# Kernel optimization log

Hardware: AMD Instinct MI355X
Metric: run time of the kernel (lower is better)

The kernel has to match this reference:

```python
import jax, jax.numpy as jnp
import numpy as np

EPS = 1e-12


def setup_inputs() -> dict:
    key = jax.random.key(0)
    k1, k2, k3 = jax.random.split(key, 3)
    N, D, K = 262144, 64, 1024
    input_data = jax.random.normal(k1, (N, D), dtype=jnp.float32)
    random_vector = jax.random.normal(k2, (N, D), dtype=jnp.float32)
    # HeUniform over (K, D): limit = sqrt(6 / fan_in) with fan_in = K
    limit = np.sqrt(6.0 / K)
    codebooks = jax.random.uniform(k3, (K, D), dtype=jnp.float32, minval=-limit, maxval=limit)
    codebooks_used = jnp.zeros((K,), dtype=jnp.int32)
    return {"input_data": input_data, "random_vector": random_vector,
            "codebooks": codebooks, "codebooks_used": codebooks_used}


def reference(input_data, random_vector, codebooks, codebooks_used):
    # training=True path of NSVQ.call
    K = codebooks.shape[0]
    N = input_data.shape[0]
    sim = input_data @ codebooks.T
    dists = (jnp.sum(input_data * input_data, axis=1, keepdims=True)
             + jnp.sum(codebooks * codebooks, axis=1)[None, :]
             - 2.0 * sim)
    min_indices = jnp.argmin(dists, axis=1)                      # [N]
    hard_q = codebooks[min_indices]                              # [N, D]
    # NSVQ noise substitution
    res_norm = jnp.sqrt(jnp.sum((input_data - hard_q) ** 2, axis=1, keepdims=True))
    rv_norm = jnp.sqrt(jnp.sum(random_vector ** 2, axis=1, keepdims=True))
    vq_error = (res_norm / (rv_norm + EPS)) * random_vector
    quantized_input = input_data + vq_error
    # perplexity from code usage histogram
    counts = jax.ops.segment_sum(jnp.ones((N,), dtype=jnp.float32), min_indices,
                                 num_segments=K)                 # [K]
    avg_probs = counts / jnp.float32(N)
    perplexity = jnp.exp(-jnp.sum(avg_probs * jnp.log(avg_probs + EPS)))
    codebooks_used_new = codebooks_used + counts.astype(jnp.int32)
    return quantized_input, perplexity, codebooks_used_new
```

## Files before the change

### kernel.cpp

```cpp
#include <hip/hip_runtime.h>
#include <math.h>


#define NROWS 262144
#define DIM 64
#define KCODES 1024
#define ND ((size_t)NROWS * DIM)

typedef __attribute__((ext_vector_type(8))) _Float16 f16x8;
typedef __attribute__((ext_vector_type(4))) float f32x4;

typedef const __attribute__((address_space(1))) void* as1p;
typedef __attribute__((address_space(3))) void* as3p;
__device__ inline void gl_lds16(const void* g, void* l) {
    __builtin_amdgcn_global_load_lds((as1p)g, (as3p)l, 16, 0, 0);
}

__global__ __launch_bounds__(256) void nsvq_prep(
    const float* __restrict__ cb, _Float16* __restrict__ cbs,
    float* __restrict__ cnorm)
{
    const int tid = blockIdx.x * 256 + threadIdx.x;
    const int k = tid >> 3;
    const int u = tid & 7;
    const float* p = cb + (size_t)k * DIM + u * 8;
    float4 f0 = *(const float4*)p;
    float4 f1 = *(const float4*)(p + 4);
    float fv[8] = {f0.x, f0.y, f0.z, f0.w, f1.x, f1.y, f1.z, f1.w};

    float s = 0.f;
    f16x8 hv, lv;
#pragma unroll
    for (int j = 0; j < 8; ++j) {
        s = fmaf(fv[j], fv[j], s);
        float m2 = -2.0f * fv[j];
        _Float16 h = (_Float16)m2;
        hv[j] = h;
        lv[j] = (_Float16)(m2 - (float)h);
    }
#pragma unroll
    for (int o = 1; o < 8; o <<= 1) s += __shfl_xor(s, o, 64);

    const size_t base = (size_t)(k >> 6) * 8192 + (size_t)u * 512 + (size_t)(k & 63) * 8;
    *(f16x8*)(cbs + base) = hv;
    *(f16x8*)(cbs + base + 4096) = lv;
    if (u == 0) cnorm[k] = s;
}

__global__ __launch_bounds__(256, 4) void nsvq_fused(
    const float* __restrict__ x, const float* __restrict__ rv,
    const _Float16* __restrict__ cbs, const float* __restrict__ cnorm,
    float* __restrict__ out, unsigned int* __restrict__ counts)
{
    __shared__ _Float16 lds[16384];

    const int tid  = threadIdx.x;
    const int lane = tid & 63;
    const int wave = tid >> 6;
    const int q    = lane >> 4;
    const int n    = lane & 15;
    const int wBase = blockIdx.x * 128 + wave * 32;

#pragma unroll
    for (int r = 0; r < 4; ++r) {
        const int off = (r * 256 + tid) * 8;
        gl_lds16(cbs + off, lds + off);
    }

    f16x8 ah[2][2], al[2][2];
    float xx[2];
#pragma unroll
    for (int s = 0; s < 2; ++s) {
        const int row = wBase + s * 16 + n;
        const float* px = x + (size_t)row * DIM + q * 8;
        float acc = 0.f;
#pragma unroll
        for (int c2 = 0; c2 < 2; ++c2) {
            float4 g0 = *(const float4*)(px + c2 * 32);
            float4 g1 = *(const float4*)(px + c2 * 32 + 4);
            float fv[8] = {g0.x, g0.y, g0.z, g0.w, g1.x, g1.y, g1.z, g1.w};
#pragma unroll
            for (int j = 0; j < 8; ++j) {
                float f = fv[j];
                acc = fmaf(f, f, acc);
                _Float16 h = (_Float16)f;
                ah[s][c2][j] = h;
                al[s][c2][j] = (_Float16)(f - (float)h);
            }
        }
        acc += __shfl_xor(acc, 16, 64);
        acc += __shfl_xor(acc, 32, 64);
        xx[s] = acc;
    }

    float cn_cur[4], cn_nxt[4];
#pragma unroll
    for (int t = 0; t < 4; ++t) cn_cur[t] = cnorm[t * 16 + n];

    float best[2][4];
    int   bidx[2][4];
#pragma unroll
    for (int s = 0; s < 2; ++s)
#pragma unroll
        for (int r = 0; r < 4; ++r) { best[s][r] = 3.4e38f; bidx[s][r] = 0; }

    __syncthreads();

    auto compute_chunk = [&](int b, int cbase) {
        const _Float16* buf = lds + b * 8192;
#pragma unroll
        for (int t = 0; t < 4; ++t) {
            const int ci = (t * 16 + n) * 8;
            f16x8 bh0 = *(const f16x8*)(buf + q * 512 + ci);
            f16x8 bh1 = *(const f16x8*)(buf + (q + 4) * 512 + ci);
            f16x8 bl0 = *(const f16x8*)(buf + 4096 + q * 512 + ci);
            f16x8 bl1 = *(const f16x8*)(buf + 4096 + (q + 4) * 512 + ci);
            const int code = cbase + t * 16 + n;
#pragma unroll
            for (int s = 0; s < 2; ++s) {
                f32x4 a = {cn_cur[t], cn_cur[t], cn_cur[t], cn_cur[t]};
                a = __builtin_amdgcn_mfma_f32_16x16x32_f16(ah[s][0], bh0, a, 0, 0, 0);
                a = __builtin_amdgcn_mfma_f32_16x16x32_f16(ah[s][1], bh1, a, 0, 0, 0);
                a = __builtin_amdgcn_mfma_f32_16x16x32_f16(al[s][0], bh0, a, 0, 0, 0);
                a = __builtin_amdgcn_mfma_f32_16x16x32_f16(al[s][1], bh1, a, 0, 0, 0);
                a = __builtin_amdgcn_mfma_f32_16x16x32_f16(ah[s][0], bl0, a, 0, 0, 0);
                a = __builtin_amdgcn_mfma_f32_16x16x32_f16(ah[s][1], bl1, a, 0, 0, 0);
#pragma unroll
                for (int r = 0; r < 4; ++r) {
                    if (a[r] < best[s][r]) { best[s][r] = a[r]; bidx[s][r] = code; }
                }
            }
        }
    };

    for (int c = 0; c < 15; ++c) {
        const int b = c & 1;
        {
            const _Float16* src = cbs + (size_t)(c + 1) * 8192;
            _Float16* dst = lds + (b ^ 1) * 8192;
#pragma unroll
            for (int r = 0; r < 4; ++r) {
                const int off = (r * 256 + tid) * 8;
                gl_lds16(src + off, dst + off);
            }
#pragma unroll
            for (int t = 0; t < 4; ++t) cn_nxt[t] = cnorm[(c + 1) * 64 + t * 16 + n];
        }
        compute_chunk(b, c * 64);
        __syncthreads();
#pragma unroll
        for (int t = 0; t < 4; ++t) cn_cur[t] = cn_nxt[t];
    }
    compute_chunk(1, 15 * 64);

#pragma unroll
    for (int o = 1; o < 16; o <<= 1) {
#pragma unroll
        for (int s = 0; s < 2; ++s)
#pragma unroll
            for (int r = 0; r < 4; ++r) {
                float od = __shfl_xor(best[s][r], o, 64);
                int   ok = __shfl_xor(bidx[s][r], o, 64);
                if (od < best[s][r] || (od == best[s][r] && ok < bidx[s][r])) {
                    best[s][r] = od; bidx[s][r] = ok;
                }
            }
    }
    if (n == 0) {
#pragma unroll
        for (int s = 0; s < 2; ++s)
#pragma unroll
            for (int r = 0; r < 4; ++r) atomicAdd(&counts[bidx[s][r]], 1u);
    }

    const int src = ((n >> 2) << 4) | n;
#pragma unroll
    for (int s = 0; s < 2; ++s) {
        float w0 = __shfl(best[s][0], src, 64);
        float w1 = __shfl(best[s][1], src, 64);
        float w2 = __shfl(best[s][2], src, 64);
        float w3 = __shfl(best[s][3], src, 64);
        float wa = (n & 1) ? w1 : w0;
        float wb = (n & 1) ? w3 : w2;
        float dmin = (n & 2) ? wb : wa;

        float res2 = xx[s] + dmin;
        if (res2 < 0.f) res2 = 0.f;
        const float resn = sqrtf(res2);

        const int row = wBase + s * 16 + n;
        const float* pr = rv + (size_t)row * DIM + q * 8;
        float rvf[16];
        float rr = 0.f;
#pragma unroll
        for (int c2 = 0; c2 < 2; ++c2) {
            float4 g0 = *(const float4*)(pr + c2 * 32);
            float4 g1 = *(const float4*)(pr + c2 * 32 + 4);
            rvf[c2 * 8 + 0] = g0.x; rvf[c2 * 8 + 1] = g0.y;
            rvf[c2 * 8 + 2] = g0.z; rvf[c2 * 8 + 3] = g0.w;
            rvf[c2 * 8 + 4] = g1.x; rvf[c2 * 8 + 5] = g1.y;
            rvf[c2 * 8 + 6] = g1.z; rvf[c2 * 8 + 7] = g1.w;
#pragma unroll
            for (int j = 0; j < 8; ++j) rr = fmaf(rvf[c2 * 8 + j], rvf[c2 * 8 + j], rr);
        }
        rr += __shfl_xor(rr, 16, 64);
        rr += __shfl_xor(rr, 32, 64);
        const float scale = resn / (sqrtf(rr) + 1e-12f);

        float* po = out + (size_t)row * DIM + q * 8;
#pragma unroll
        for (int c2 = 0; c2 < 2; ++c2) {
            float4 o0, o1;
            o0.x = fmaf(scale, rvf[c2 * 8 + 0], (float)ah[s][c2][0] + (float)al[s][c2][0]);
            o0.y = fmaf(scale, rvf[c2 * 8 + 1], (float)ah[s][c2][1] + (float)al[s][c2][1]);
            o0.z = fmaf(scale, rvf[c2 * 8 + 2], (float)ah[s][c2][2] + (float)al[s][c2][2]);
            o0.w = fmaf(scale, rvf[c2 * 8 + 3], (float)ah[s][c2][3] + (float)al[s][c2][3]);
            o1.x = fmaf(scale, rvf[c2 * 8 + 4], (float)ah[s][c2][4] + (float)al[s][c2][4]);
            o1.y = fmaf(scale, rvf[c2 * 8 + 5], (float)ah[s][c2][5] + (float)al[s][c2][5]);
            o1.z = fmaf(scale, rvf[c2 * 8 + 6], (float)ah[s][c2][6] + (float)al[s][c2][6]);
            o1.w = fmaf(scale, rvf[c2 * 8 + 7], (float)ah[s][c2][7] + (float)al[s][c2][7]);
            *(float4*)(po + c2 * 32) = o0;
            *(float4*)(po + c2 * 32 + 4) = o1;
        }
    }
}

__global__ void nsvq_finalize(const unsigned int* __restrict__ counts,
                              const int* __restrict__ used,
                              float* __restrict__ out)
{
    const int k = threadIdx.x;
    const unsigned c = counts[k];
    float avg = (float)c * (1.0f / (float)NROWS);
    float term = (c > 0) ? (-avg * logf(avg + 1e-12f)) : 0.0f;

    float v = term;
#pragma unroll
    for (int o = 32; o > 0; o >>= 1) v += __shfl_down(v, o, 64);

    __shared__ float partial[16];
    if ((threadIdx.x & 63) == 0) partial[threadIdx.x >> 6] = v;
    __syncthreads();

    if (threadIdx.x < 64) {
        float s = (threadIdx.x < 16) ? partial[threadIdx.x] : 0.0f;
#pragma unroll
        for (int o = 32; o > 0; o >>= 1) s += __shfl_down(s, o, 64);
        if (threadIdx.x == 0) out[ND] = expf(s);
    }
    out[ND + 1 + k] = (float)(c + (unsigned)used[k]);
}

extern "C" void kernel_launch(void* const* d_in, const int* in_sizes, int n_in,
                              void* d_out, int out_size, void* d_ws, size_t ws_size,
                              hipStream_t stream) {
    const float* x    = (const float*)d_in[0];
    const float* rv   = (const float*)d_in[1];
    const float* cb   = (const float*)d_in[2];
    const int*   used = (const int*)d_in[3];
    float* out = (float*)d_out;

    char* ws = (char*)d_ws;
    unsigned int* counts = (unsigned int*)ws;
    float*        cnorm  = (float*)(ws + 4096);
    _Float16*     cbs    = (_Float16*)(ws + 8192);

    hipMemsetAsync(counts, 0, KCODES * sizeof(unsigned int), stream);
    nsvq_prep<<<KCODES * 8 / 256, 256, 0, stream>>>(cb, cbs, cnorm);
    nsvq_fused<<<NROWS / 128, 256, 0, stream>>>(x, rv, cbs, cnorm, out, counts);
    nsvq_finalize<<<1, KCODES, 0, stream>>>(counts, used, out);
}
```

Measured before the change: 264.0 us.

## Triple-buffer codebook LDS pipeline, stage norms in LDS, fold memset into prep

Replaces the double-buffered codebook streaming with a three-buffer ring that prefetches two chunks ahead. Each chunk ends with a counted vmcnt wait and a raw barrier instead of __syncthreads, and the loop is fully unrolled with setprio around the MFMA section. Codebook norms are loaded once into LDS instead of per chunk from global memory. The counts memset is folded into the prep kernel, dropping one launch. LDS use grows from 32 KB to about 52 KB per block, which may lower occupancy below the requested 4 blocks, and the hand-placed vmcnt values have to stay in step with the number of outstanding loads.

```diff
diff --git a/kernel.cpp b/kernel.cpp
--- a/kernel.cpp
+++ b/kernel.cpp
@@ -18,9 +18,10 @@
 
 __global__ __launch_bounds__(256) void nsvq_prep(
     const float* __restrict__ cb, _Float16* __restrict__ cbs,
-    float* __restrict__ cnorm)
+    float* __restrict__ cnorm, unsigned int* __restrict__ counts)
 {
     const int tid = blockIdx.x * 256 + threadIdx.x;
+    if (tid < KCODES) counts[tid] = 0u;
     const int k = tid >> 3;
     const int u = tid & 7;
     const float* p = cb + (size_t)k * DIM + u * 8;
@@ -52,7 +53,8 @@
     const _Float16* __restrict__ cbs, const float* __restrict__ cnorm,
     float* __restrict__ out, unsigned int* __restrict__ counts)
 {
-    __shared__ _Float16 lds[16384];
+    __shared__ _Float16 lds[3 * 8192 + 2048];
+    float* cnf = (float*)(lds + 3 * 8192);
 
     const int tid  = threadIdx.x;
     const int lane = tid & 63;
@@ -61,12 +63,6 @@
     const int n    = lane & 15;
     const int wBase = blockIdx.x * 128 + wave * 32;
 
-#pragma unroll
-    for (int r = 0; r < 4; ++r) {
-        const int off = (r * 256 + tid) * 8;
-        gl_lds16(cbs + off, lds + off);
-    }
-
     f16x8 ah[2][2], al[2][2];
     float xx[2];
 #pragma unroll
@@ -93,9 +89,17 @@
         xx[s] = acc;
     }
 
-    float cn_cur[4], cn_nxt[4];
-#pragma unroll
-    for (int t = 0; t < 4; ++t) cn_cur[t] = cnorm[t * 16 + n];
+    gl_lds16(cnorm + tid * 4, cnf + tid * 4);
+#pragma unroll
+    for (int r = 0; r < 4; ++r) {
+        const int off = (r * 256 + tid) * 8;
+        gl_lds16(cbs + off, lds + off);
+    }
+#pragma unroll
+    for (int r = 0; r < 4; ++r) {
+        const int off = (r * 256 + tid) * 8;
+        gl_lds16(cbs + 8192 + off, lds + 8192 + off);
+    }
 
     float best[2][4];
     int   bidx[2][4];
@@ -104,10 +108,29 @@
 #pragma unroll
         for (int r = 0; r < 4; ++r) { best[s][r] = 3.4e38f; bidx[s][r] = 0; }
 
-    __syncthreads();
-
-    auto compute_chunk = [&](int b, int cbase) {
-        const _Float16* buf = lds + b * 8192;
+    asm volatile("s_waitcnt vmcnt(4)" ::: "memory");
+    __builtin_amdgcn_s_barrier();
+    __builtin_amdgcn_sched_barrier(0);
+
+#pragma unroll
+    for (int c = 0; c < 16; ++c) {
+        const _Float16* buf = lds + (c % 3) * 8192;
+
+        if (c < 14) {
+            const _Float16* src = cbs + (size_t)(c + 2) * 8192;
+            _Float16* dst = lds + ((c + 2) % 3) * 8192;
+#pragma unroll
+            for (int r = 0; r < 4; ++r) {
+                const int off = (r * 256 + tid) * 8;
+                gl_lds16(src + off, dst + off);
+            }
+        }
+
+        float cn[4];
+#pragma unroll
+        for (int t = 0; t < 4; ++t) cn[t] = cnf[c * 64 + t * 16 + n];
+
+        __builtin_amdgcn_s_setprio(1);
 #pragma unroll
         for (int t = 0; t < 4; ++t) {
             const int ci = (t * 16 + n) * 8;
@@ -115,10 +138,10 @@
             f16x8 bh1 = *(const f16x8*)(buf + (q + 4) * 512 + ci);
             f16x8 bl0 = *(const f16x8*)(buf + 4096 + q * 512 + ci);
             f16x8 bl1 = *(const f16x8*)(buf + 4096 + (q + 4) * 512 + ci);
-            const int code = cbase + t * 16 + n;
+            const int code = c * 64 + t * 16 + n;
 #pragma unroll
             for (int s = 0; s < 2; ++s) {
-                f32x4 a = {cn_cur[t], cn_cur[t], cn_cur[t], cn_cur[t]};
+                f32x4 a = {cn[t], cn[t], cn[t], cn[t]};
                 a = __builtin_amdgcn_mfma_f32_16x16x32_f16(ah[s][0], bh0, a, 0, 0, 0);
                 a = __builtin_amdgcn_mfma_f32_16x16x32_f16(ah[s][1], bh1, a, 0, 0, 0);
                 a = __builtin_amdgcn_mfma_f32_16x16x32_f16(al[s][0], bh0, a, 0, 0, 0);
@@ -131,27 +154,15 @@
                 }
             }
         }
-    };
-
-    for (int c = 0; c < 15; ++c) {
-        const int b = c & 1;
-        {
-            const _Float16* src = cbs + (size_t)(c + 1) * 8192;
-            _Float16* dst = lds + (b ^ 1) * 8192;
-#pragma unroll
-            for (int r = 0; r < 4; ++r) {
-                const int off = (r * 256 + tid) * 8;
-                gl_lds16(src + off, dst + off);
-            }
-#pragma unroll
-            for (int t = 0; t < 4; ++t) cn_nxt[t] = cnorm[(c + 1) * 64 + t * 16 + n];
-        }
-        compute_chunk(b, c * 64);
-        __syncthreads();
-#pragma unroll
-        for (int t = 0; t < 4; ++t) cn_cur[t] = cn_nxt[t];
-    }
-    compute_chunk(1, 15 * 64);
+        __builtin_amdgcn_s_setprio(0);
+
+        if (c < 15) {
+            if (c < 14) asm volatile("s_waitcnt vmcnt(4)" ::: "memory");
+            else        asm volatile("s_waitcnt vmcnt(0)" ::: "memory");
+            __builtin_amdgcn_s_barrier();
+            __builtin_amdgcn_sched_barrier(0);
+        }
+    }
 
 #pragma unroll
     for (int o = 1; o < 16; o <<= 1) {
@@ -265,8 +276,7 @@
     float*        cnorm  = (float*)(ws + 4096);
     _Float16*     cbs    = (_Float16*)(ws + 8192);
 
-    hipMemsetAsync(counts, 0, KCODES * sizeof(unsigned int), stream);
-    nsvq_prep<<<KCODES * 8 / 256, 256, 0, stream>>>(cb, cbs, cnorm);
+    nsvq_prep<<<KCODES * 8 / 256, 256, 0, stream>>>(cb, cbs, cnorm, counts);
     nsvq_fused<<<NROWS / 128, 256, 0, stream>>>(x, rv, cbs, cnorm, out, counts);
     nsvq_finalize<<<1, KCODES, 0, stream>>>(counts, used, out);
 }
```

After: 425.9 us. +61.3%, slower.
